# Kernel tuning notes

Hardware: AMD Instinct MI355X
Metric: run time of the kernel (lower is better)

Reference implementation:

```python
import jax, jax.numpy as jnp
import numpy as np

N = 100000
C_IN = 128
C_OUT = 128
N_EDGE_TYPE = 7
N_SAMPLES = 2
E = 700000


def setup_inputs() -> dict:
    key = jax.random.key(0)
    k1, k2, k3, k4 = jax.random.split(key, 4)
    x = jax.random.normal(k1, (N, C_IN), dtype=jnp.float32)
    col = jax.random.randint(k2, (E,), 0, N, dtype=jnp.int64)
    # per-edge slot index = row * n_edge_type + edge_type, sorted (select_k_sorted needs sorted idx)
    index_sorted = jnp.sort(jax.random.randint(k3, (E,), 0, N * N_EDGE_TYPE, dtype=jnp.int64))
    weights = jax.random.normal(k4, (N_EDGE_TYPE * C_IN, C_OUT), dtype=jnp.float32)
    return {"x": x, "col": col, "index_sorted": index_sorted, "weights": weights}


def reference(x, col, index_sorted, weights):
    n, c = x.shape
    S = n * N_EDGE_TYPE  # total (node, edge_type) slots
    # group stats over the sorted slot index (replaces unique_consecutive + counts)
    counts = jax.ops.segment_sum(jnp.ones_like(index_sorted, dtype=jnp.int32),
                                 index_sorted, num_segments=S)
    starts = jnp.cumsum(counts) - counts  # first edge position of each slot
    # Monte Carlo: sample N_SAMPLES edges (with replacement) per slot
    rel = jax.random.randint(jax.random.key(42), (S, N_SAMPLES), 0, 1 << 30, dtype=jnp.int32)
    rel = rel % jnp.maximum(counts, 1)[:, None]
    gidx = starts[:, None] + rel              # [S, k] indices into the edge list
    x_col = x[col]                            # [E, C] neighbor features
    gathered = x_col[gidx]                    # [S, k, C]
    gathered = jnp.where((counts > 0)[:, None, None], gathered, jnp.zeros((), x.dtype))
    col_data = gathered.mean(axis=1)          # [S, C]
    # self slot (edge_type = n_edge_type-1) is overwritten with the node's own feature
    self_idx = jnp.arange(n) * N_EDGE_TYPE + (N_EDGE_TYPE - 1)
    col_data = col_data.at[self_idx].set(x)
    return col_data.reshape(n, N_EDGE_TYPE * c) @ weights
```

## Files before the change

kernel.cpp:

```cpp
#include <hip/hip_runtime.h>
#include <hip/hip_bf16.h>
#include <stdint.h>

#define N_NODES 100000
#define C 128
#define NET 7
#define E_EDGES 700000
#define S_SLOTS (N_NODES * NET)
#define BM 64
#define NB_CVTX 6250
#define NB_CVTW 56
#define NB_PAIRS ((S_SLOTS + 255) / 256)

typedef __attribute__((ext_vector_type(8))) short short8;
typedef __attribute__((ext_vector_type(4))) float f32x4;
typedef __attribute__((ext_vector_type(4))) unsigned int uint4v;

struct TF2 { uint32_t a, b; };

__host__ __device__ constexpr uint32_t rotl32c(uint32_t v, int r) {
    return (v << r) | (v >> (32 - r));
}

__host__ __device__ constexpr TF2 threefry2x32(uint32_t k0, uint32_t k1,
                                               uint32_t x0, uint32_t x1) {
    const uint32_t ks0 = k0, ks1 = k1, ks2 = 0x1BD11BDAu ^ k0 ^ k1;
    x0 += ks0; x1 += ks1;
#define RND(r) { x0 += x1; x1 = rotl32c(x1, (r)); x1 ^= x0; }
    RND(13) RND(15) RND(26) RND(6)
    x0 += ks1; x1 += ks2 + 1u;
    RND(17) RND(29) RND(16) RND(24)
    x0 += ks2; x1 += ks0 + 2u;
    RND(13) RND(15) RND(26) RND(6)
    x0 += ks0; x1 += ks1 + 3u;
    RND(17) RND(29) RND(16) RND(24)
    x0 += ks1; x1 += ks2 + 4u;
    RND(13) RND(15) RND(26) RND(6)
    x0 += ks2; x1 += ks0 + 5u;
#undef RND
    return TF2{x0, x1};
}

constexpr TF2 K2 = threefry2x32(0u, 42u, 0u, 1u);

__device__ __forceinline__ uint32_t jax_bits32(uint32_t f) {
    TF2 o = threefry2x32(K2.a, K2.b, 0u, f);
    return o.a ^ o.b;
}

__device__ __forceinline__ unsigned short f2bf(float f) {
    uint32_t u = __float_as_uint(f);
    u += 0x7fffu + ((u >> 16) & 1u);
    return (unsigned short)(u >> 16);
}

__device__ __forceinline__ uint32_t sumpack(uint32_t a, uint32_t b) {
    float alo = __uint_as_float(a << 16);
    float ahi = __uint_as_float(a & 0xffff0000u);
    float blo = __uint_as_float(b << 16);
    float bhi = __uint_as_float(b & 0xffff0000u);
    return (__float_as_uint(ahi + bhi) & 0xffff0000u) | (__float_as_uint(alo + blo) >> 16);
}

__device__ __forceinline__ uint4v sumpack4(uint4v a, uint4v b) {
    uint4v o;
    o.x = sumpack(a.x, b.x); o.y = sumpack(a.y, b.y);
    o.z = sumpack(a.z, b.z); o.w = sumpack(a.w, b.w);
    return o;
}

__device__ __forceinline__ int lbound(const int* __restrict__ idx, int v) {
    int l = 0, r = E_EDGES;
    while (l < r) { int m = (l + r) >> 1; if (idx[m] < v) l = m + 1; else r = m; }
    return l;
}

__global__ __launch_bounds__(256) void prep(const float* __restrict__ x,
                                            const int* __restrict__ col,
                                            const int* __restrict__ idx,
                                            const float* __restrict__ W,
                                            unsigned short* __restrict__ xb,
                                            unsigned short* __restrict__ Wf,
                                            int2* __restrict__ pairs) {
    const int b = blockIdx.x;
    if (b < NB_CVTX) {
        int i = b * 256 + threadIdx.x;
        const float4* src = (const float4*)x + (size_t)i * 2;
        float4 a = src[0], v = src[1];
        union { unsigned short u[8]; uint4v q; } o;
        o.u[0] = f2bf(a.x); o.u[1] = f2bf(a.y); o.u[2] = f2bf(a.z); o.u[3] = f2bf(a.w);
        o.u[4] = f2bf(v.x); o.u[5] = f2bf(v.y); o.u[6] = f2bf(v.z); o.u[7] = f2bf(v.w);
        ((uint4v*)xb)[i] = o.q;
    } else if (b < NB_CVTX + NB_CVTW) {
        int t = (b - NB_CVTX) * 256 + threadIdx.x;
        int l = t & 63, ks = (t >> 6) & 3, n16 = (t >> 8) & 7, et = t >> 11;
        int n = n16 * 16 + (l & 15);
        int k0 = ks * 32 + (l >> 4) * 8;
        union { unsigned short u[8]; uint4v q; } o;
#pragma unroll
        for (int j = 0; j < 8; j++)
            o.u[j] = f2bf(0.5f * W[(size_t)(et * 128 + k0 + j) * 128 + n]);
        ((uint4v*)Wf)[t] = o.q;
    } else {
        int s = (b - NB_CVTX - NB_CVTW) * 256 + threadIdx.x;
        bool valid = s < S_SLOTS;
        int lo = E_EDGES;
        if (valid) lo = lbound(idx, s);
        int hi = __shfl_down(lo, 1);
        if ((threadIdx.x & 63) == 63 && valid)
            hi = (s + 1 < S_SLOTS) ? lbound(idx, s + 1) : E_EDGES;
        if (!valid) return;
        if (s % NET == NET - 1) {
            int node = s / NET;
            pairs[s] = make_int2(node, node);
            return;
        }
        int cnt = hi - lo;
        if (cnt <= 0) { pairs[s] = make_int2(-1, -1); return; }
        uint32_t b0 = jax_bits32((uint32_t)s * 2u + 0u) & 0x3FFFFFFFu;
        uint32_t b1 = jax_bits32((uint32_t)s * 2u + 1u) & 0x3FFFFFFFu;
        pairs[s] = make_int2(col[lo + (int)(b0 % (uint32_t)cnt)],
                             col[lo + (int)(b1 % (uint32_t)cnt)]);
    }
}

__global__ __launch_bounds__(512, 4) void fused_mfma(const unsigned short* __restrict__ xb,
                                                     const int2* __restrict__ pairs,
                                                     const unsigned short* __restrict__ Wf,
                                                     float* __restrict__ out) {
    __shared__ unsigned char Alds[2][BM * 256];
    const int tid  = threadIdx.x;
    const int nb   = blockIdx.x * BM;
    const int wave = tid >> 6, lane = tid & 63;
    const int wr   = wave >> 2, wc = wave & 3;
    const int lr   = lane & 15, lg = lane >> 4;
    const char* xbc = (const char*)xb;

    const int srow = tid >> 3;
    const int c0   = (tid & 7) * 2;
    const int arow = nb + srow;
    const int prow = (arow < N_NODES) ? arow * NET : -1;
    const int sa0  = srow * 256 + (((c0    ) ^ (srow & 7)) << 4);
    const int sa1  = srow * 256 + (((c0 | 1) ^ (srow & 7)) << 4);

    uint4v g0[2][2], g1[2][2];
    int2 sp[2];

#define GLOAD(SET, PV) { \
    int2 p_ = (PV); \
    if (p_.x >= 0) { \
        const uint4v* s0_ = (const uint4v*)(xbc + ((size_t)p_.x << 8) + (c0 << 4)); \
        const uint4v* s1_ = (const uint4v*)(xbc + ((size_t)p_.y << 8) + (c0 << 4)); \
        g0[SET][0] = s0_[0]; g0[SET][1] = s0_[1]; \
        g1[SET][0] = s1_[0]; g1[SET][1] = s1_[1]; \
    } else { \
        uint4v z_ = {0u, 0u, 0u, 0u}; \
        g0[SET][0] = z_; g0[SET][1] = z_; g1[SET][0] = z_; g1[SET][1] = z_; } }

#define COMBINE(SET, BUF) { \
    uint4v v0_ = sumpack4(g0[SET][0], g1[SET][0]); \
    uint4v v1_ = sumpack4(g0[SET][1], g1[SET][1]); \
    *(uint4v*)(&Alds[BUF][sa0]) = v0_; \
    *(uint4v*)(&Alds[BUF][sa1]) = v1_; }

#define LOADB(ET) { _Pragma("unroll") \
    for (int fn_ = 0; fn_ < 2; fn_++) { _Pragma("unroll") \
        for (int ks_ = 0; ks_ < 4; ks_++) \
            bfr[fn_][ks_] = *(const short8*)(Wf \
                + (size_t)((((ET) * 8 + wc * 2 + fn_) * 4 + ks_) * 512) + lane * 8); } }

#define BARRIER() { \
    asm volatile("s_waitcnt lgkmcnt(0)" ::: "memory"); \
    __builtin_amdgcn_s_barrier(); \
    __builtin_amdgcn_sched_barrier(0); }

    f32x4 acc[2][2];
#pragma unroll
    for (int i = 0; i < 2; i++)
#pragma unroll
        for (int j = 0; j < 2; j++) acc[i][j] = (f32x4)0.f;

    short8 bfr[2][4];

    GLOAD(0, (prow >= 0) ? pairs[prow + 0] : make_int2(-1, -1))
    GLOAD(1, (prow >= 0) ? pairs[prow + 1] : make_int2(-1, -1))
    LOADB(0)
    sp[0] = (prow >= 0) ? pairs[prow + 2] : make_int2(-1, -1);
    sp[1] = (prow >= 0) ? pairs[prow + 3] : make_int2(-1, -1);
    COMBINE(0, 0)
    BARRIER()

#pragma unroll
    for (int et = 0; et < NET; ++et) {
        const int cur = et & 1;

        if (et + 2 < NET) {
            GLOAD(cur, sp[cur])
            sp[cur] = (et + 4 < NET && prow >= 0) ? pairs[prow + et + 4]
                                                  : make_int2(-1, -1);
        }
        if (et > 0) LOADB(et)

        if (et + 1 < NET) COMBINE(cur ^ 1, cur ^ 1)

#pragma unroll
        for (int ks = 0; ks < 4; ks++) {
            const int coff = ((ks * 4 + lg) ^ (lr & 7)) << 4;
            short8 a0 = *(const short8*)(&Alds[cur][(wr * 32      + lr) * 256 + coff]);
            short8 a1 = *(const short8*)(&Alds[cur][(wr * 32 + 16 + lr) * 256 + coff]);
            acc[0][0] = __builtin_amdgcn_mfma_f32_16x16x32_bf16(a0, bfr[0][ks], acc[0][0], 0, 0, 0);
            acc[0][1] = __builtin_amdgcn_mfma_f32_16x16x32_bf16(a0, bfr[1][ks], acc[0][1], 0, 0, 0);
            acc[1][0] = __builtin_amdgcn_mfma_f32_16x16x32_bf16(a1, bfr[0][ks], acc[1][0], 0, 0, 0);
            acc[1][1] = __builtin_amdgcn_mfma_f32_16x16x32_bf16(a1, bfr[1][ks], acc[1][1], 0, 0, 0);
        }

        if (et + 1 < NET) BARRIER()
    }

#pragma unroll
    for (int fm = 0; fm < 2; fm++) {
        int row0 = nb + wr * 32 + fm * 16 + lg * 4;
#pragma unroll
        for (int fn = 0; fn < 2; fn++) {
            int colo = wc * 32 + fn * 16 + lr;
#pragma unroll
            for (int j = 0; j < 4; j++)
                if (row0 + j < N_NODES)
                    out[(size_t)(row0 + j) * C + colo] = acc[fm][fn][j];
        }
    }
#undef GLOAD
#undef COMBINE
#undef LOADB
#undef BARRIER
}

extern "C" void kernel_launch(void* const* d_in, const int* in_sizes, int n_in,
                              void* d_out, int out_size, void* d_ws, size_t ws_size,
                              hipStream_t stream) {
    const float* x   = (const float*)d_in[0];
    const int*   col = (const int*)d_in[1];
    const int*   idx = (const int*)d_in[2];
    const float* W   = (const float*)d_in[3];
    float* out = (float*)d_out;

    int2* pairs        = (int2*)d_ws;
    unsigned short* xb = (unsigned short*)((char*)pairs + (size_t)S_SLOTS * 8);
    unsigned short* Wf = xb + (size_t)N_NODES * C;

    prep<<<NB_CVTX + NB_CVTW + NB_PAIRS, 256, 0, stream>>>(x, col, idx, W, xb, Wf, pairs);
    fused_mfma<<<(N_NODES + BM - 1) / BM, 512, 0, stream>>>(xb, pairs, Wf, out);
}
```

Baseline: 92.59 us.

## Replace per-slot binary search with edge-parallel segment detection; retile MFMA waves

Slot boundaries are no longer found with two binary searches per slot over the sorted index. Instead, a first kernel initializes every pair to empty or to the self pair, and a second edge-parallel kernel has each segment's first edge scan forward to get the count and sample the columns. The MFMA kernel now gives each wave 64 rows by 16 columns, so only one B fragment set is loaded per edge type and it is double-buffered. All 7 pair indices are prefetched up front and gathers use triple buffering. This costs an extra kernel launch and a serial forward scan per segment, and it changes register pressure in the main kernel.

```diff
diff --git a/kernel.cpp b/kernel.cpp
--- a/kernel.cpp
+++ b/kernel.cpp
@@ -10,7 +10,7 @@
 #define BM 64
 #define NB_CVTX 6250
 #define NB_CVTW 56
-#define NB_PAIRS ((S_SLOTS + 255) / 256)
+#define NB_INIT ((S_SLOTS + 255) / 256)
 
 typedef __attribute__((ext_vector_type(8))) short short8;
 typedef __attribute__((ext_vector_type(4))) float f32x4;
@@ -69,19 +69,11 @@
     return o;
 }
 
-__device__ __forceinline__ int lbound(const int* __restrict__ idx, int v) {
-    int l = 0, r = E_EDGES;
-    while (l < r) { int m = (l + r) >> 1; if (idx[m] < v) l = m + 1; else r = m; }
-    return l;
-}
-
-__global__ __launch_bounds__(256) void prep(const float* __restrict__ x,
-                                            const int* __restrict__ col,
-                                            const int* __restrict__ idx,
-                                            const float* __restrict__ W,
-                                            unsigned short* __restrict__ xb,
-                                            unsigned short* __restrict__ Wf,
-                                            int2* __restrict__ pairs) {
+__global__ __launch_bounds__(256) void prep1(const float* __restrict__ x,
+                                             const float* __restrict__ W,
+                                             unsigned short* __restrict__ xb,
+                                             unsigned short* __restrict__ Wf,
+                                             int2* __restrict__ pairs) {
     const int b = blockIdx.x;
     if (b < NB_CVTX) {
         int i = b * 256 + threadIdx.x;
@@ -103,25 +95,27 @@
         ((uint4v*)Wf)[t] = o.q;
     } else {
         int s = (b - NB_CVTX - NB_CVTW) * 256 + threadIdx.x;
-        bool valid = s < S_SLOTS;
-        int lo = E_EDGES;
-        if (valid) lo = lbound(idx, s);
-        int hi = __shfl_down(lo, 1);
-        if ((threadIdx.x & 63) == 63 && valid)
-            hi = (s + 1 < S_SLOTS) ? lbound(idx, s + 1) : E_EDGES;
-        if (!valid) return;
-        if (s % NET == NET - 1) {
-            int node = s / NET;
-            pairs[s] = make_int2(node, node);
-            return;
-        }
-        int cnt = hi - lo;
-        if (cnt <= 0) { pairs[s] = make_int2(-1, -1); return; }
-        uint32_t b0 = jax_bits32((uint32_t)s * 2u + 0u) & 0x3FFFFFFFu;
-        uint32_t b1 = jax_bits32((uint32_t)s * 2u + 1u) & 0x3FFFFFFFu;
-        pairs[s] = make_int2(col[lo + (int)(b0 % (uint32_t)cnt)],
-                             col[lo + (int)(b1 % (uint32_t)cnt)]);
+        if (s >= S_SLOTS) return;
+        int node = s / NET;
+        pairs[s] = (s - node * NET == NET - 1) ? make_int2(node, node)
+                                               : make_int2(-1, -1);
     }
+}
+
+__global__ __launch_bounds__(256) void prep2(const int* __restrict__ idx,
+                                             const int* __restrict__ col,
+                                             int2* __restrict__ pairs) {
+    int e = blockIdx.x * 256 + threadIdx.x;
+    if (e >= E_EDGES) return;
+    int s = idx[e];
+    if (e > 0 && idx[e - 1] == s) return;
+    int len = 1;
+    while (e + len < E_EDGES && idx[e + len] == s) ++len;
+    if (s % NET == NET - 1) return;
+    uint32_t b0 = jax_bits32((uint32_t)s * 2u + 0u) & 0x3FFFFFFFu;
+    uint32_t b1 = jax_bits32((uint32_t)s * 2u + 1u) & 0x3FFFFFFFu;
+    pairs[s] = make_int2(col[e + (int)(b0 % (uint32_t)len)],
+                         col[e + (int)(b1 % (uint32_t)len)]);
 }
 
 __global__ __launch_bounds__(512, 4) void fused_mfma(const unsigned short* __restrict__ xb,
@@ -132,27 +126,28 @@
     const int tid  = threadIdx.x;
     const int nb   = blockIdx.x * BM;
     const int wave = tid >> 6, lane = tid & 63;
-    const int wr   = wave >> 2, wc = wave & 3;
     const int lr   = lane & 15, lg = lane >> 4;
     const char* xbc = (const char*)xb;
 
     const int srow = tid >> 3;
-    const int c0   = (tid & 7) * 2;
+    const int q16  = (tid & 7) * 16;
     const int arow = nb + srow;
     const int prow = (arow < N_NODES) ? arow * NET : -1;
-    const int sa0  = srow * 256 + (((c0    ) ^ (srow & 7)) << 4);
-    const int sa1  = srow * 256 + (((c0 | 1) ^ (srow & 7)) << 4);
-
-    uint4v g0[2][2], g1[2][2];
-    int2 sp[2];
+    const int sa0  = srow * 256 + ((q16 >> 4) ^ (srow & 7)) * 16;
+    const int sa1  = sa0 + 128;
+
+    uint4v g0[3][2], g1[3][2];
+    short8 bfr[2][4];
 
 #define GLOAD(SET, PV) { \
     int2 p_ = (PV); \
     if (p_.x >= 0) { \
-        const uint4v* s0_ = (const uint4v*)(xbc + ((size_t)p_.x << 8) + (c0 << 4)); \
-        const uint4v* s1_ = (const uint4v*)(xbc + ((size_t)p_.y << 8) + (c0 << 4)); \
-        g0[SET][0] = s0_[0]; g0[SET][1] = s0_[1]; \
-        g1[SET][0] = s1_[0]; g1[SET][1] = s1_[1]; \
+        const char* b0_ = xbc + ((size_t)p_.x << 8); \
+        const char* b1_ = xbc + ((size_t)p_.y << 8); \
+        g0[SET][0] = *(const uint4v*)(b0_ + q16); \
+        g0[SET][1] = *(const uint4v*)(b0_ + 128 + q16); \
+        g1[SET][0] = *(const uint4v*)(b1_ + q16); \
+        g1[SET][1] = *(const uint4v*)(b1_ + 128 + q16); \
     } else { \
         uint4v z_ = {0u, 0u, 0u, 0u}; \
         g0[SET][0] = z_; g0[SET][1] = z_; g1[SET][0] = z_; g1[SET][1] = z_; } }
@@ -163,71 +158,65 @@
     *(uint4v*)(&Alds[BUF][sa0]) = v0_; \
     *(uint4v*)(&Alds[BUF][sa1]) = v1_; }
 
-#define LOADB(ET) { _Pragma("unroll") \
-    for (int fn_ = 0; fn_ < 2; fn_++) { _Pragma("unroll") \
-        for (int ks_ = 0; ks_ < 4; ks_++) \
-            bfr[fn_][ks_] = *(const short8*)(Wf \
-                + (size_t)((((ET) * 8 + wc * 2 + fn_) * 4 + ks_) * 512) + lane * 8); } }
+#define LOADB(DST, ET) { _Pragma("unroll") \
+    for (int ks_ = 0; ks_ < 4; ks_++) \
+        (DST)[ks_] = *(const short8*)(Wf \
+            + (size_t)((((ET) * 8 + wave) * 4 + ks_) * 512) + lane * 8); }
 
 #define BARRIER() { \
     asm volatile("s_waitcnt lgkmcnt(0)" ::: "memory"); \
     __builtin_amdgcn_s_barrier(); \
     __builtin_amdgcn_sched_barrier(0); }
 
-    f32x4 acc[2][2];
-#pragma unroll
-    for (int i = 0; i < 2; i++)
-#pragma unroll
-        for (int j = 0; j < 2; j++) acc[i][j] = (f32x4)0.f;
-
-    short8 bfr[2][4];
-
-    GLOAD(0, (prow >= 0) ? pairs[prow + 0] : make_int2(-1, -1))
-    GLOAD(1, (prow >= 0) ? pairs[prow + 1] : make_int2(-1, -1))
-    LOADB(0)
-    sp[0] = (prow >= 0) ? pairs[prow + 2] : make_int2(-1, -1);
-    sp[1] = (prow >= 0) ? pairs[prow + 3] : make_int2(-1, -1);
+    f32x4 acc[4];
+#pragma unroll
+    for (int i = 0; i < 4; i++) acc[i] = (f32x4)0.f;
+
+    int2 pj[7];
+#pragma unroll
+    for (int j = 0; j < 7; j++)
+        pj[j] = (prow >= 0) ? pairs[prow + j] : make_int2(-1, -1);
+
+    GLOAD(0, pj[0])
+    GLOAD(1, pj[1])
+    GLOAD(2, pj[2])
+    LOADB(bfr[0], 0)
     COMBINE(0, 0)
+    GLOAD(0, pj[3])
     BARRIER()
 
 #pragma unroll
     for (int et = 0; et < NET; ++et) {
         const int cur = et & 1;
 
-        if (et + 2 < NET) {
-            GLOAD(cur, sp[cur])
-            sp[cur] = (et + 4 < NET && prow >= 0) ? pairs[prow + et + 4]
-                                                  : make_int2(-1, -1);
-        }
-        if (et > 0) LOADB(et)
-
-        if (et + 1 < NET) COMBINE(cur ^ 1, cur ^ 1)
+        if (et + 1 < NET) LOADB(bfr[cur ^ 1], et + 1)
+
+        if (et >= 1 && et + 3 < NET) GLOAD(et % 3, pj[et + 3])
+
+        if (et + 1 < NET) COMBINE((et + 1) % 3, cur ^ 1)
 
 #pragma unroll
         for (int ks = 0; ks < 4; ks++) {
-            const int coff = ((ks * 4 + lg) ^ (lr & 7)) << 4;
-            short8 a0 = *(const short8*)(&Alds[cur][(wr * 32      + lr) * 256 + coff]);
-            short8 a1 = *(const short8*)(&Alds[cur][(wr * 32 + 16 + lr) * 256 + coff]);
-            acc[0][0] = __builtin_amdgcn_mfma_f32_16x16x32_bf16(a0, bfr[0][ks], acc[0][0], 0, 0, 0);
-            acc[0][1] = __builtin_amdgcn_mfma_f32_16x16x32_bf16(a0, bfr[1][ks], acc[0][1], 0, 0, 0);
-            acc[1][0] = __builtin_amdgcn_mfma_f32_16x16x32_bf16(a1, bfr[0][ks], acc[1][0], 0, 0, 0);
-            acc[1][1] = __builtin_amdgcn_mfma_f32_16x16x32_bf16(a1, bfr[1][ks], acc[1][1], 0, 0, 0);
+            const int coff = (((ks * 4 + lg) ^ (lr & 7)) << 4);
+            short8 b_ = bfr[cur][ks];
+#pragma unroll
+            for (int fm = 0; fm < 4; fm++) {
+                short8 a_ = *(const short8*)(&Alds[cur][(fm * 16 + lr) * 256 + coff]);
+                acc[fm] = __builtin_amdgcn_mfma_f32_16x16x32_bf16(a_, b_, acc[fm], 0, 0, 0);
+            }
         }
 
         if (et + 1 < NET) BARRIER()
     }
 
 #pragma unroll
-    for (int fm = 0; fm < 2; fm++) {
-        int row0 = nb + wr * 32 + fm * 16 + lg * 4;
-#pragma unroll
-        for (int fn = 0; fn < 2; fn++) {
-            int colo = wc * 32 + fn * 16 + lr;
-#pragma unroll
-            for (int j = 0; j < 4; j++)
-                if (row0 + j < N_NODES)
-                    out[(size_t)(row0 + j) * C + colo] = acc[fm][fn][j];
-        }
+    for (int fm = 0; fm < 4; fm++) {
+        int row0 = nb + fm * 16 + lg * 4;
+        int colo = wave * 16 + lr;
+#pragma unroll
+        for (int j = 0; j < 4; j++)
+            if (row0 + j < N_NODES)
+                out[(size_t)(row0 + j) * C + colo] = acc[fm][j];
     }
 #undef GLOAD
 #undef COMBINE
@@ -248,6 +237,7 @@
     unsigned short* xb = (unsigned short*)((char*)pairs + (size_t)S_SLOTS * 8);
     unsigned short* Wf = xb + (size_t)N_NODES * C;
 
-    prep<<<NB_CVTX + NB_CVTW + NB_PAIRS, 256, 0, stream>>>(x, col, idx, W, xb, Wf, pairs);
+    prep1<<<NB_CVTX + NB_CVTW + NB_INIT, 256, 0, stream>>>(x, W, xb, Wf, pairs);
+    prep2<<<(E_EDGES + 255) / 256, 256, 0, stream>>>(idx, col, pairs);
     fused_mfma<<<(N_NODES + BM - 1) / BM, 512, 0, stream>>>(xb, pairs, Wf, out);
 }
```

New measurement: 75.01 us. 19.0% less time.
